# Kernel optimization log

Hardware: AMD Instinct MI355X
Metric: run time of the kernel (lower is better)

The kernel has to match this reference:

```python
import jax, jax.numpy as jnp
import numpy as np

EMBED_DIM = 1024
NUM_HEADS = 16
HEAD_DIM = EMBED_DIM // NUM_HEADS


def setup_inputs() -> dict:
    key = jax.random.key(0)
    k1, k2, k3, k4, k5 = jax.random.split(key, 5)
    C = EMBED_DIM
    x = jax.random.normal(k1, (4, 2048, C), dtype=jnp.float32)
    s = 1.0 / np.sqrt(C)
    qkv_w = jax.random.uniform(k2, (3 * C, C), jnp.float32, -s, s)
    qkv_b = jax.random.uniform(k3, (3 * C,), jnp.float32, -s, s)
    proj_w = jax.random.uniform(k4, (C, C), jnp.float32, -s, s)
    proj_b = jax.random.uniform(k5, (C,), jnp.float32, -s, s)
    return {"x": x, "qkv_w": qkv_w, "qkv_b": qkv_b, "proj_w": proj_w, "proj_b": proj_b}


def reference(x, qkv_w, qkv_b, proj_w, proj_b):
    B, T, C = x.shape
    H, D = NUM_HEADS, HEAD_DIM
    qkv = jnp.einsum('btc,oc->bto', x, qkv_w) + qkv_b  # [B,T,3C]
    q, k, v = jnp.split(qkv, 3, axis=2)
    # [B,T,C] -> [B,H,T,D]
    q = q.reshape(B, T, H, D).transpose(0, 2, 1, 3)
    k = k.reshape(B, T, H, D).transpose(0, 2, 1, 3)
    v = v.reshape(B, T, H, D).transpose(0, 2, 1, 3)
    scores = jnp.einsum('bhqd,bhkd->bhqk', q, k) / jnp.sqrt(jnp.float32(D)).astype(q.dtype)
    causal = jnp.tril(jnp.ones((T, T), dtype=bool))
    scores = jnp.where(causal[None, None], scores, jnp.finfo(scores.dtype).min)
    attn = jax.nn.softmax(scores, axis=-1)
    out = jnp.einsum('bhqk,bhkd->bhqd', attn, v)
    out = out.transpose(0, 2, 1, 3).reshape(B, T, C)
    return jnp.einsum('btc,oc->bto', out, proj_w) + proj_b
```

## Files before the change

kernel.cpp:

```cpp
#include <hip/hip_runtime.h>

#define EMBED 1024
#define C3    3072
#define NHEAD 16
#define HDIM  64
#define BB    4
#define TT    2048
#define MTOK  8192

typedef __bf16 bf16;
typedef __bf16 bf16x4 __attribute__((ext_vector_type(4)));
typedef __bf16 bf16x8 __attribute__((ext_vector_type(8)));
typedef float  f32x4  __attribute__((ext_vector_type(4)));
typedef float  f32x16 __attribute__((ext_vector_type(16)));
typedef unsigned int u32;

__device__ __forceinline__ void gload_lds16(const bf16* g, bf16* l) {
  __builtin_amdgcn_global_load_lds((__attribute__((address_space(1))) void*)g,
                                   (__attribute__((address_space(3))) void*)l,
                                   16, 0, 0);
}

__device__ __forceinline__ u32 pkbf(float lo, float hi_) {
  union { bf16 h[2]; u32 w; } u;
  u.h[0] = (bf16)lo; u.h[1] = (bf16)hi_;
  return u.w;
}

union upw { u32 w[4]; bf16x8 v; };

__global__ __launch_bounds__(256) void cvt_all(const float* __restrict__ x,
                                               const float* __restrict__ w1,
                                               const float* __restrict__ w2,
                                               bf16* __restrict__ xb,
                                               bf16* __restrict__ wqkv,
                                               bf16* __restrict__ wproj) {
  const int N1 = MTOK * EMBED, N2 = C3 * EMBED, N3 = EMBED * EMBED;
  int i = (blockIdx.x * blockDim.x + threadIdx.x) * 4;
  const float* src; bf16* dst;
  if (i < N1)           { src = x + i;            dst = xb + i; }
  else if (i < N1 + N2) { src = w1 + (i - N1);    dst = wqkv + (i - N1); }
  else if (i < N1 + N2 + N3) { src = w2 + (i - N1 - N2); dst = wproj + (i - N1 - N2); }
  else return;
  float4 v = *reinterpret_cast<const float4*>(src);
  bf16x4 o;
  o[0] = (bf16)v.x; o[1] = (bf16)v.y; o[2] = (bf16)v.z; o[3] = (bf16)v.w;
  *reinterpret_cast<bf16x4*>(dst) = o;
}

__device__ __forceinline__ void gemm_core(const bf16* __restrict__ A,
                                          const bf16* __restrict__ W,
                                          int K, int bm0, int bn0,
                                          int wm, int wn, int l15, int lg,
                                          f32x4 (&acc)[4][4]) {
  __shared__ __align__(16) bf16 lA[128 * 64];
  __shared__ __align__(16) bf16 lB[128 * 64];
  const int tid  = threadIdx.x;
  const int grow = tid >> 3;
  const int gseg = tid & 7;

  const bf16* srcA[4];
  const bf16* srcB[4];
#pragma unroll
  for (int r = 0; r < 4; ++r) {
    const int row = r * 32 + grow;
    const int seg = gseg ^ (row & 7);
    srcA[r] = A + (size_t)(bm0 + row) * K + seg * 8;
    srcB[r] = W + (size_t)(bn0 + row) * K + seg * 8;
  }
  int offA[2][4], offB[2][4];
#pragma unroll
  for (int kk = 0; kk < 2; ++kk) {
#pragma unroll
    for (int i = 0; i < 4; ++i) {
      const int rowA = wm + i * 16 + l15;
      const int rowB = wn + i * 16 + l15;
      offA[kk][i] = rowA * 128 + ((kk * 64 + lg * 16) ^ ((rowA & 7) << 4));
      offB[kk][i] = rowB * 128 + ((kk * 64 + lg * 16) ^ ((rowB & 7) << 4));
    }
  }

  for (int kt = 0; kt < K; kt += 64) {
#pragma unroll
    for (int r = 0; r < 4; ++r) {
      gload_lds16(srcA[r] + kt, &lA[(r * 256 + tid) * 8]);
      gload_lds16(srcB[r] + kt, &lB[(r * 256 + tid) * 8]);
    }
    __syncthreads();
    const char* Ab = (const char*)lA;
    const char* Bb = (const char*)lB;
#pragma unroll
    for (int kk = 0; kk < 2; ++kk) {
      bf16x8 af[4], bf_[4];
#pragma unroll
      for (int i = 0; i < 4; ++i) af[i]  = *reinterpret_cast<const bf16x8*>(Ab + offA[kk][i]);
#pragma unroll
      for (int j = 0; j < 4; ++j) bf_[j] = *reinterpret_cast<const bf16x8*>(Bb + offB[kk][j]);
#pragma unroll
      for (int i = 0; i < 4; ++i)
#pragma unroll
        for (int j = 0; j < 4; ++j)
          acc[i][j] = __builtin_amdgcn_mfma_f32_16x16x32_bf16(af[i], bf_[j],
                                                              acc[i][j], 0, 0, 0);
    }
    __syncthreads();
  }
}

__global__ __launch_bounds__(256) void gemm_qkv(const bf16* __restrict__ A,
                                                const bf16* __restrict__ W,
                                                const float* __restrict__ bias,
                                                bf16* __restrict__ Qh,
                                                bf16* __restrict__ Kh,
                                                bf16* __restrict__ VhT) {
  const int tid  = threadIdx.x;
  const int lane = tid & 63, wave = tid >> 6;
  const int wm   = (wave >> 1) * 64;
  const int wn   = (wave & 1) * 64;
  const int bn0  = blockIdx.x * 128;
  const int bm0  = blockIdx.y * 128;
  const int l15  = lane & 15, lg = lane >> 4;

  f32x4 acc[4][4] = {};
  gemm_core(A, W, EMBED, bm0, bn0, wm, wn, l15, lg, acc);

  const int sec = bn0 >> 10;
#pragma unroll
  for (int i = 0; i < 4; ++i)
#pragma unroll
    for (int j = 0; j < 4; ++j) {
      const int col = bn0 + wn + j * 16 + l15;
      const float bs = bias[col];
      const int c2 = col & 1023, hh = c2 >> 6, dd = c2 & 63;
      const int rowb = bm0 + wm + i * 16 + lg * 4;
      const int bb = rowb >> 11, t0 = rowb & 2047;
      const int bh = bb * 16 + hh;
      if (sec < 2) {
        bf16* dst = (sec ? Kh : Qh) + ((size_t)bh * TT + t0) * HDIM + dd;
#pragma unroll
        for (int r = 0; r < 4; ++r) dst[(size_t)r * HDIM] = (bf16)(acc[i][j][r] + bs);
      } else {
        bf16x4 o4;
#pragma unroll
        for (int r = 0; r < 4; ++r) o4[r] = (bf16)(acc[i][j][r] + bs);
        *reinterpret_cast<bf16x4*>(VhT + ((size_t)bh * HDIM + dd) * TT + t0) = o4;
      }
    }
}

__global__ __launch_bounds__(256) void gemm_bt(const bf16* __restrict__ A,
                                               const bf16* __restrict__ W,
                                               const float* __restrict__ bias,
                                               float* __restrict__ Cf,
                                               int M, int N, int K) {
  const int tid  = threadIdx.x;
  const int lane = tid & 63, wave = tid >> 6;
  const int wm   = (wave >> 1) * 64;
  const int wn   = (wave & 1) * 64;
  const int bn0  = blockIdx.x * 128;
  const int bm0  = blockIdx.y * 128;
  const int l15  = lane & 15, lg = lane >> 4;

  f32x4 acc[4][4] = {};
  gemm_core(A, W, K, bm0, bn0, wm, wn, l15, lg, acc);

#pragma unroll
  for (int i = 0; i < 4; ++i)
#pragma unroll
    for (int j = 0; j < 4; ++j) {
      int col = bn0 + wn + j * 16 + l15;
      float bs = bias[col];
#pragma unroll
      for (int r = 0; r < 4; ++r) {
        int row = bm0 + wm + i * 16 + lg * 4 + r;
        Cf[(size_t)row * N + col] = acc[i][j][r] + bs;
      }
    }
}

__device__ __forceinline__ void attn_tile(const char* kbase, const char* vbase,
                                          const bf16x8 (&qfr)[4], f32x16 (&oacc)[2],
                                          float& mrun, float& srun,
                                          const int kv0, const int q0w,
                                          const int l31, const int hi, const int swz) {
  f32x16 s0 = {}, s1 = {};
  __builtin_amdgcn_s_setprio(1);
#pragma unroll
  for (int dc = 0; dc < 4; ++dc) {
    bf16x8 kf = *reinterpret_cast<const bf16x8*>(
        kbase + l31 * 128 + (((2 * dc + hi) * 16) ^ swz));
    s0 = __builtin_amdgcn_mfma_f32_32x32x16_bf16(kf, qfr[dc], s0, 0, 0, 0);
  }
#pragma unroll
  for (int dc = 0; dc < 4; ++dc) {
    bf16x8 kf = *reinterpret_cast<const bf16x8*>(
        kbase + (32 + l31) * 128 + (((2 * dc + hi) * 16) ^ swz));
    s1 = __builtin_amdgcn_mfma_f32_32x32x16_bf16(kf, qfr[dc], s1, 0, 0, 0);
  }
  __builtin_amdgcn_s_setprio(0);

  if (kv0 + 63 > q0w) {
    const int qg = q0w + l31;
#pragma unroll
    for (int r = 0; r < 16; ++r) {
      const int kvb = kv0 + (r & 3) + 8 * (r >> 2) + 4 * hi;
      if (kvb > qg)      s0[r] = -3e38f;
      if (kvb + 32 > qg) s1[r] = -3e38f;
    }
  }

  float m8[8];
#pragma unroll
  for (int i = 0; i < 8; ++i)
    m8[i] = fmaxf(fmaxf(s0[i], s0[i + 8]), fmaxf(s1[i], s1[i + 8]));
#pragma unroll
  for (int st = 4; st > 0; st >>= 1)
#pragma unroll
    for (int i = 0; i < st; ++i) m8[i] = fmaxf(m8[i], m8[i + st]);
  float mx = fmaxf(m8[0], __shfl_xor(m8[0], 32));

  float mref = mrun;
  if (!__all(mx <= mrun + 8.0f)) {
    const float mnew = fmaxf(mrun, mx);
    const float corr = __builtin_amdgcn_exp2f(mrun - mnew);
    mrun = mnew; mref = mnew;
    srun *= corr;
#pragma unroll
    for (int r = 0; r < 16; ++r) { oacc[0][r] *= corr; oacc[1][r] *= corr; }
  }

  float psum = 0.0f;
#pragma unroll
  for (int r = 0; r < 16; ++r) {
    s0[r] = __builtin_amdgcn_exp2f(s0[r] - mref);
    s1[r] = __builtin_amdgcn_exp2f(s1[r] - mref);
    psum += s0[r] + s1[r];
  }
  srun += psum;

  upw pw[4];
#pragma unroll
  for (int cl = 0; cl < 2; ++cl) {
    {
      u32 a01 = pkbf(s0[8 * cl + 0], s0[8 * cl + 1]);
      u32 a23 = pkbf(s0[8 * cl + 2], s0[8 * cl + 3]);
      u32 b01 = pkbf(s0[8 * cl + 4], s0[8 * cl + 5]);
      u32 b23 = pkbf(s0[8 * cl + 6], s0[8 * cl + 7]);
      asm("v_permlane32_swap_b32 %0, %1" : "+v"(a01), "+v"(b01));
      asm("v_permlane32_swap_b32 %0, %1" : "+v"(a23), "+v"(b23));
      pw[cl].w[0] = a01; pw[cl].w[1] = a23; pw[cl].w[2] = b01; pw[cl].w[3] = b23;
    }
    {
      u32 a01 = pkbf(s1[8 * cl + 0], s1[8 * cl + 1]);
      u32 a23 = pkbf(s1[8 * cl + 2], s1[8 * cl + 3]);
      u32 b01 = pkbf(s1[8 * cl + 4], s1[8 * cl + 5]);
      u32 b23 = pkbf(s1[8 * cl + 6], s1[8 * cl + 7]);
      asm("v_permlane32_swap_b32 %0, %1" : "+v"(a01), "+v"(b01));
      asm("v_permlane32_swap_b32 %0, %1" : "+v"(a23), "+v"(b23));
      pw[2 + cl].w[0] = a01; pw[2 + cl].w[1] = a23; pw[2 + cl].w[2] = b01; pw[2 + cl].w[3] = b23;
    }
  }

  __builtin_amdgcn_s_setprio(1);
#pragma unroll
  for (int dh = 0; dh < 2; ++dh) {
    const char* vrow = vbase + (32 * dh + l31) * 128;
#pragma unroll
    for (int c = 0; c < 4; ++c) {
      bf16x8 vf = *reinterpret_cast<const bf16x8*>(vrow + (((2 * c + hi) * 16) ^ swz));
      oacc[dh] = __builtin_amdgcn_mfma_f32_32x32x16_bf16(vf, pw[c].v, oacc[dh], 0, 0, 0);
    }
  }
  __builtin_amdgcn_s_setprio(0);
}

__global__ __launch_bounds__(256, 2) void attn_kernel(const bf16* __restrict__ Qh,
                                                      const bf16* __restrict__ Kh,
                                                      const bf16* __restrict__ VhT,
                                                      bf16* __restrict__ aout) {
  __shared__ __align__(16) bf16 lK[2][64 * 64];
  __shared__ __align__(16) bf16 lVT[2][64 * 64];
  const int tid  = threadIdx.x;
  const int lane = tid & 63, wave = tid >> 6;
  const int l31  = lane & 31;
  const int hi   = lane >> 5;
  const int bid  = blockIdx.x;
  const int bh   = bid & 63;
  const int p    = bid >> 6;
  const int qtH  = 15 - p, qtL = p;
  const int b    = bh >> 4, h = bh & 15;
  const int q0H  = qtH * 128 + wave * 32;
  const int q0L  = qtL * 128 + wave * 32;
  const size_t tb = (size_t)b * TT;
  const int swz  = (l31 & 7) << 4;

  const float QSCALE = 0.18033688011112042f;
  bf16x8 qfrH[4], qfrL[4];
  {
    const bf16* qrowH = Qh + ((size_t)bh * TT + q0H + l31) * HDIM;
    const bf16* qrowL = Qh + ((size_t)bh * TT + q0L + l31) * HDIM;
#pragma unroll
    for (int dc = 0; dc < 4; ++dc) {
      bf16x8 vH = *reinterpret_cast<const bf16x8*>(qrowH + dc * 16 + hi * 8);
      bf16x8 vL = *reinterpret_cast<const bf16x8*>(qrowL + dc * 16 + hi * 8);
      bf16x8 oH, oL;
#pragma unroll
      for (int j = 0; j < 8; ++j) {
        oH[j] = (bf16)((float)vH[j] * QSCALE);
        oL[j] = (bf16)((float)vL[j] * QSCALE);
      }
      qfrH[dc] = oH; qfrL[dc] = oL;
    }
  }

  f32x16 oaccH[2] = {}, oaccL[2] = {};
  float mH = -3e38f, sH = 0.0f, mL = -3e38f, sL = 0.0f;

  const int r0 = tid >> 3, sg = tid & 7;
  const bf16* kS0 = Kh + ((size_t)bh * TT + r0) * HDIM + (size_t)(sg ^ (r0 & 7)) * 8;
  const bf16* kS1 = Kh + ((size_t)bh * TT + 32 + r0) * HDIM + (size_t)(sg ^ (r0 & 7)) * 8;
  const bf16* vS0 = VhT + ((size_t)bh * HDIM + r0) * TT + (size_t)(sg ^ (r0 & 7)) * 8;
  const bf16* vS1 = VhT + ((size_t)bh * HDIM + 32 + r0) * TT + (size_t)(sg ^ (r0 & 7)) * 8;

  const int nkv = 2 * qtH + 2;

  gload_lds16(kS0, &lK[0][tid * 8]);
  gload_lds16(kS1, &lK[0][(tid + 256) * 8]);
  gload_lds16(vS0, &lVT[0][tid * 8]);
  gload_lds16(vS1, &lVT[0][(tid + 256) * 8]);
  __syncthreads();

  int cur = 0;
  for (int t = 0; t < nkv; ++t) {
    const int kv0 = t * 64;
    if (t + 1 < nkv) {
      const int kvn = kv0 + 64;
      gload_lds16(kS0 + (size_t)kvn * HDIM, &lK[cur ^ 1][tid * 8]);
      gload_lds16(kS1 + (size_t)kvn * HDIM, &lK[cur ^ 1][(tid + 256) * 8]);
      gload_lds16(vS0 + kvn, &lVT[cur ^ 1][tid * 8]);
      gload_lds16(vS1 + kvn, &lVT[cur ^ 1][(tid + 256) * 8]);
    }

    const char* kbase = (const char*)&lK[cur][0];
    const char* vbase = (const char*)&lVT[cur][0];
    if (kv0 <= q0H + 31)
      attn_tile(kbase, vbase, qfrH, oaccH, mH, sH, kv0, q0H, l31, hi, swz);
    if (kv0 <= q0L + 31)
      attn_tile(kbase, vbase, qfrL, oaccL, mL, sL, kv0, q0L, l31, hi, swz);

    __syncthreads();
    cur ^= 1;
  }

#pragma unroll
  for (int band = 0; band < 2; ++band) {
    const f32x16* oacc = band ? oaccL : oaccH;
    float sr = band ? sL : sH;
    sr += __shfl_xor(sr, 32);
    const float inv = 1.0f / sr;
    const int q = (band ? q0L : q0H) + l31;
    bf16* orow = aout + (tb + q) * (size_t)EMBED + h * HDIM;
#pragma unroll
    for (int dh = 0; dh < 2; ++dh)
#pragma unroll
      for (int rb = 0; rb < 4; ++rb) {
        bf16x4 o4;
#pragma unroll
        for (int k = 0; k < 4; ++k) o4[k] = (bf16)(oacc[dh][4 * rb + k] * inv);
        *reinterpret_cast<bf16x4*>(orow + 32 * dh + 8 * rb + 4 * hi) = o4;
      }
  }
}

extern "C" void kernel_launch(void* const* d_in, const int* in_sizes, int n_in,
                              void* d_out, int out_size, void* d_ws, size_t ws_size,
                              hipStream_t stream) {
  const float* x      = (const float*)d_in[0];
  const float* qkv_w  = (const float*)d_in[1];
  const float* qkv_b  = (const float*)d_in[2];
  const float* proj_w = (const float*)d_in[3];
  const float* proj_b = (const float*)d_in[4];
  float* out = (float*)d_out;

  const size_t QSZ = (size_t)BB * NHEAD * TT * HDIM;
  char* ws = (char*)d_ws;
  bf16* xb    = (bf16*)ws;
  bf16* wqkv  = xb + (size_t)MTOK * EMBED;
  bf16* wproj = wqkv + (size_t)C3 * EMBED;
  bf16* Qh    = wproj + (size_t)EMBED * EMBED;
  bf16* Kh    = Qh + QSZ;
  bf16* VhT   = Kh + QSZ;
  bf16* aob   = xb;

  const int NCVT = (MTOK * EMBED + C3 * EMBED + EMBED * EMBED) / 4;
  cvt_all<<<dim3((NCVT + 255) / 256), dim3(256), 0, stream>>>(x, qkv_w, proj_w,
                                                              xb, wqkv, wproj);

  gemm_qkv<<<dim3(C3 / 128, MTOK / 128), dim3(256), 0, stream>>>(xb, wqkv, qkv_b, Qh, Kh, VhT);

  attn_kernel<<<dim3(512), dim3(256), 0, stream>>>(Qh, Kh, VhT, aob);

  gemm_bt<<<dim3(EMBED / 128, MTOK / 128), dim3(256), 0, stream>>>(
      aob, wproj, proj_b, out, MTOK, EMBED, EMBED);
}
```

Baseline: 165.7 us.

## Split attention blocks into two 64-row halves with 128 threads each

Each attention block now has 2 waves instead of 4 and covers 64 query rows per band, so the grid doubles to 1024 blocks. The K/V tile loads are reorganized so 128 threads issue four 16-row groups per buffer. The goal is more blocks to fill the GPU's compute units and finer load balancing across the causal workload. In exchange, each K/V tile is loaded from global memory twice as often, since two blocks now share each query tile.

```diff
diff --git a/kernel.cpp b/kernel.cpp
--- a/kernel.cpp
+++ b/kernel.cpp
@@ -274,7 +274,7 @@
   __builtin_amdgcn_s_setprio(0);
 }
 
-__global__ __launch_bounds__(256, 2) void attn_kernel(const bf16* __restrict__ Qh,
+__global__ __launch_bounds__(128, 2) void attn_kernel(const bf16* __restrict__ Qh,
                                                       const bf16* __restrict__ Kh,
                                                       const bf16* __restrict__ VhT,
                                                       bf16* __restrict__ aout) {
@@ -285,12 +285,13 @@
   const int l31  = lane & 31;
   const int hi   = lane >> 5;
   const int bid  = blockIdx.x;
-  const int bh   = bid & 63;
-  const int p    = bid >> 6;
+  const int qh   = bid & 1;
+  const int bh   = (bid >> 1) & 63;
+  const int p    = bid >> 7;
   const int qtH  = 15 - p, qtL = p;
   const int b    = bh >> 4, h = bh & 15;
-  const int q0H  = qtH * 128 + wave * 32;
-  const int q0L  = qtL * 128 + wave * 32;
+  const int q0H  = qtH * 128 + qh * 64 + wave * 32;
+  const int q0L  = qtL * 128 + qh * 64 + wave * 32;
   const size_t tb = (size_t)b * TT;
   const int swz  = (l31 & 7) << 4;
 
@@ -316,18 +317,24 @@
   f32x16 oaccH[2] = {}, oaccL[2] = {};
   float mH = -3e38f, sH = 0.0f, mL = -3e38f, sL = 0.0f;
 
-  const int r0 = tid >> 3, sg = tid & 7;
-  const bf16* kS0 = Kh + ((size_t)bh * TT + r0) * HDIM + (size_t)(sg ^ (r0 & 7)) * 8;
-  const bf16* kS1 = Kh + ((size_t)bh * TT + 32 + r0) * HDIM + (size_t)(sg ^ (r0 & 7)) * 8;
-  const bf16* vS0 = VhT + ((size_t)bh * HDIM + r0) * TT + (size_t)(sg ^ (r0 & 7)) * 8;
-  const bf16* vS1 = VhT + ((size_t)bh * HDIM + 32 + r0) * TT + (size_t)(sg ^ (r0 & 7)) * 8;
+  const int r0 = tid >> 3;
+  const int sg = tid & 7;
+  const int seg = sg ^ (r0 & 7);
+  const bf16* kS[4];
+  const bf16* vS[4];
+#pragma unroll
+  for (int g = 0; g < 4; ++g) {
+    kS[g] = Kh + ((size_t)bh * TT + g * 16 + r0) * HDIM + seg * 8;
+    vS[g] = VhT + ((size_t)bh * HDIM + g * 16 + r0) * TT + seg * 8;
+  }
 
   const int nkv = 2 * qtH + 2;
 
-  gload_lds16(kS0, &lK[0][tid * 8]);
-  gload_lds16(kS1, &lK[0][(tid + 256) * 8]);
-  gload_lds16(vS0, &lVT[0][tid * 8]);
-  gload_lds16(vS1, &lVT[0][(tid + 256) * 8]);
+#pragma unroll
+  for (int g = 0; g < 4; ++g) {
+    gload_lds16(kS[g], &lK[0][(g * 128 + tid) * 8]);
+    gload_lds16(vS[g], &lVT[0][(g * 128 + tid) * 8]);
+  }
   __syncthreads();
 
   int cur = 0;
@@ -335,10 +342,11 @@
     const int kv0 = t * 64;
     if (t + 1 < nkv) {
       const int kvn = kv0 + 64;
-      gload_lds16(kS0 + (size_t)kvn * HDIM, &lK[cur ^ 1][tid * 8]);
-      gload_lds16(kS1 + (size_t)kvn * HDIM, &lK[cur ^ 1][(tid + 256) * 8]);
-      gload_lds16(vS0 + kvn, &lVT[cur ^ 1][tid * 8]);
-      gload_lds16(vS1 + kvn, &lVT[cur ^ 1][(tid + 256) * 8]);
+#pragma unroll
+      for (int g = 0; g < 4; ++g) {
+        gload_lds16(kS[g] + (size_t)kvn * HDIM, &lK[cur ^ 1][(g * 128 + tid) * 8]);
+        gload_lds16(vS[g] + kvn, &lVT[cur ^ 1][(g * 128 + tid) * 8]);
+      }
     }
 
     const char* kbase = (const char*)&lK[cur][0];
@@ -398,7 +406,7 @@
 
   gemm_qkv<<<dim3(C3 / 128, MTOK / 128), dim3(256), 0, stream>>>(xb, wqkv, qkv_b, Qh, Kh, VhT);
 
-  attn_kernel<<<dim3(512), dim3(256), 0, stream>>>(Qh, Kh, VhT, aob);
+  attn_kernel<<<dim3(1024), dim3(128), 0, stream>>>(Qh, Kh, VhT, aob);
 
   gemm_bt<<<dim3(EMBED / 128, MTOK / 128), dim3(256), 0, stream>>>(
       aob, wproj, proj_b, out, MTOK, EMBED, EMBED);
```

Result: no change. 168.8 us (+1.8%).

## Software-pipeline attention so QK of next tile overlaps softmax and PV

Applied to the files above, without the earlier changes.

Splits the per-tile attention work into a QK MFMA stage and a softmax/PV stage. Each iteration computes the scores for tile t while finishing softmax and the PV product for tile t-1, using ping-pong score registers. The K/V LDS ring grows from two to four slots so tile t-1's V stays valid while later tiles are staged. The aim is to hide the softmax latency behind matrix-core work, at the cost of twice the LDS per block and many more live score VGPRs, which may cause spills or lower occupancy.

```diff
diff --git a/kernel.cpp b/kernel.cpp
--- a/kernel.cpp
+++ b/kernel.cpp
@@ -178,27 +178,32 @@
     }
 }
 
-__device__ __forceinline__ void attn_tile(const char* kbase, const char* vbase,
-                                          const bf16x8 (&qfr)[4], f32x16 (&oacc)[2],
-                                          float& mrun, float& srun,
-                                          const int kv0, const int q0w,
-                                          const int l31, const int hi, const int swz) {
-  f32x16 s0 = {}, s1 = {};
+__device__ __forceinline__ void load_kf(const char* kbase, bf16x8 (&kf0)[4], bf16x8 (&kf1)[4],
+                                        int l31, int hi, int swz) {
+#pragma unroll
+  for (int dc = 0; dc < 4; ++dc) {
+    kf0[dc] = *reinterpret_cast<const bf16x8*>(kbase + l31 * 128 + (((2 * dc + hi) * 16) ^ swz));
+    kf1[dc] = *reinterpret_cast<const bf16x8*>(kbase + (32 + l31) * 128 + (((2 * dc + hi) * 16) ^ swz));
+  }
+}
+
+__device__ __forceinline__ void qk_one(const bf16x8 (&kf0)[4], const bf16x8 (&kf1)[4],
+                                       const bf16x8 (&qfr)[4], f32x16& s0, f32x16& s1) {
+  f32x16 a = {}, b = {};
   __builtin_amdgcn_s_setprio(1);
 #pragma unroll
   for (int dc = 0; dc < 4; ++dc) {
-    bf16x8 kf = *reinterpret_cast<const bf16x8*>(
-        kbase + l31 * 128 + (((2 * dc + hi) * 16) ^ swz));
-    s0 = __builtin_amdgcn_mfma_f32_32x32x16_bf16(kf, qfr[dc], s0, 0, 0, 0);
-  }
-#pragma unroll
-  for (int dc = 0; dc < 4; ++dc) {
-    bf16x8 kf = *reinterpret_cast<const bf16x8*>(
-        kbase + (32 + l31) * 128 + (((2 * dc + hi) * 16) ^ swz));
-    s1 = __builtin_amdgcn_mfma_f32_32x32x16_bf16(kf, qfr[dc], s1, 0, 0, 0);
+    a = __builtin_amdgcn_mfma_f32_32x32x16_bf16(kf0[dc], qfr[dc], a, 0, 0, 0);
+    b = __builtin_amdgcn_mfma_f32_32x32x16_bf16(kf1[dc], qfr[dc], b, 0, 0, 0);
   }
   __builtin_amdgcn_s_setprio(0);
-
+  s0 = a; s1 = b;
+}
+
+__device__ __forceinline__ void fin_band(const char* vbase, f32x16& s0, f32x16& s1,
+                                         f32x16 (&oacc)[2], float& mrun, float& srun,
+                                         const int kv0, const int q0w,
+                                         const int l31, const int hi, const int swz) {
   if (kv0 + 63 > q0w) {
     const int qg = q0w + l31;
 #pragma unroll
@@ -208,7 +213,6 @@
       if (kvb + 32 > qg) s1[r] = -3e38f;
     }
   }
-
   float m8[8];
 #pragma unroll
   for (int i = 0; i < 8; ++i)
@@ -274,12 +278,21 @@
   __builtin_amdgcn_s_setprio(0);
 }
 
+__device__ __forceinline__ void stage_tile(const bf16* kS0, const bf16* kS1,
+                                           const bf16* vS0, const bf16* vS1,
+                                           int kv, bf16* kb, bf16* vb, int tid) {
+  gload_lds16(kS0 + (size_t)kv * HDIM, kb + tid * 8);
+  gload_lds16(kS1 + (size_t)kv * HDIM, kb + (tid + 256) * 8);
+  gload_lds16(vS0 + kv, vb + tid * 8);
+  gload_lds16(vS1 + kv, vb + (tid + 256) * 8);
+}
+
 __global__ __launch_bounds__(256, 2) void attn_kernel(const bf16* __restrict__ Qh,
                                                       const bf16* __restrict__ Kh,
                                                       const bf16* __restrict__ VhT,
                                                       bf16* __restrict__ aout) {
-  __shared__ __align__(16) bf16 lK[2][64 * 64];
-  __shared__ __align__(16) bf16 lVT[2][64 * 64];
+  __shared__ __align__(16) bf16 lK[4][64 * 64];
+  __shared__ __align__(16) bf16 lVT[4][64 * 64];
   const int tid  = threadIdx.x;
   const int lane = tid & 63, wave = tid >> 6;
   const int l31  = lane & 31;
@@ -314,7 +327,7 @@
   }
 
   f32x16 oaccH[2] = {}, oaccL[2] = {};
-  float mH = -3e38f, sH = 0.0f, mL = -3e38f, sL = 0.0f;
+  float mH = -3e38f, sHr = 0.0f, mL = -3e38f, sLr = 0.0f;
 
   const int r0 = tid >> 3, sg = tid & 7;
   const bf16* kS0 = Kh + ((size_t)bh * TT + r0) * HDIM + (size_t)(sg ^ (r0 & 7)) * 8;
@@ -324,38 +337,62 @@
 
   const int nkv = 2 * qtH + 2;
 
-  gload_lds16(kS0, &lK[0][tid * 8]);
-  gload_lds16(kS1, &lK[0][(tid + 256) * 8]);
-  gload_lds16(vS0, &lVT[0][tid * 8]);
-  gload_lds16(vS1, &lVT[0][(tid + 256) * 8]);
+  f32x16 sAh0, sAh1, sAl0, sAl1;
+  f32x16 sBh0, sBh1, sBl0, sBl1;
+
+#define HALF_ITER(T, NH0, NH1, NL0, NL1, OH0, OH1, OL0, OL1)                              \
+  do {                                                                                    \
+    const int t_ = (T);                                                                   \
+    if (t_ + 1 < nkv)                                                                     \
+      stage_tile(kS0, kS1, vS0, vS1, (t_ + 1) * 64,                                       \
+                 &lK[(t_ + 1) & 3][0], &lVT[(t_ + 1) & 3][0], tid);                       \
+    {                                                                                     \
+      const char* vb_ = (const char*)&lVT[(t_ - 1) & 3][0];                               \
+      const int pk_ = (t_ - 1) * 64;                                                      \
+      fin_band(vb_, OH0, OH1, oaccH, mH, sHr, pk_, q0H, l31, hi, swz);                    \
+      if (pk_ <= q0L + 31)                                                                \
+        fin_band(vb_, OL0, OL1, oaccL, mL, sLr, pk_, q0L, l31, hi, swz);                  \
+    }                                                                                     \
+    {                                                                                     \
+      const char* kb_ = (const char*)&lK[t_ & 3][0];                                      \
+      bf16x8 kf0_[4], kf1_[4];                                                            \
+      load_kf(kb_, kf0_, kf1_, l31, hi, swz);                                             \
+      qk_one(kf0_, kf1_, qfrH, NH0, NH1);                                                 \
+      if (t_ * 64 <= q0L + 31) qk_one(kf0_, kf1_, qfrL, NL0, NL1);                        \
+    }                                                                                     \
+    __syncthreads();                                                                      \
+  } while (0)
+
+  stage_tile(kS0, kS1, vS0, vS1, 0, &lK[0][0], &lVT[0][0], tid);
   __syncthreads();
-
-  int cur = 0;
-  for (int t = 0; t < nkv; ++t) {
-    const int kv0 = t * 64;
-    if (t + 1 < nkv) {
-      const int kvn = kv0 + 64;
-      gload_lds16(kS0 + (size_t)kvn * HDIM, &lK[cur ^ 1][tid * 8]);
-      gload_lds16(kS1 + (size_t)kvn * HDIM, &lK[cur ^ 1][(tid + 256) * 8]);
-      gload_lds16(vS0 + kvn, &lVT[cur ^ 1][tid * 8]);
-      gload_lds16(vS1 + kvn, &lVT[cur ^ 1][(tid + 256) * 8]);
-    }
-
-    const char* kbase = (const char*)&lK[cur][0];
-    const char* vbase = (const char*)&lVT[cur][0];
-    if (kv0 <= q0H + 31)
-      attn_tile(kbase, vbase, qfrH, oaccH, mH, sH, kv0, q0H, l31, hi, swz);
-    if (kv0 <= q0L + 31)
-      attn_tile(kbase, vbase, qfrL, oaccL, mL, sL, kv0, q0L, l31, hi, swz);
-
+  {
+    stage_tile(kS0, kS1, vS0, vS1, 64, &lK[1][0], &lVT[1][0], tid);
+    bf16x8 kf0_[4], kf1_[4];
+    load_kf((const char*)&lK[0][0], kf0_, kf1_, l31, hi, swz);
+    qk_one(kf0_, kf1_, qfrH, sAh0, sAh1);
+    qk_one(kf0_, kf1_, qfrL, sAl0, sAl1);
     __syncthreads();
-    cur ^= 1;
-  }
+  }
+
+  int t = 1;
+  for (; t + 1 < nkv; t += 2) {
+    HALF_ITER(t,     sBh0, sBh1, sBl0, sBl1, sAh0, sAh1, sAl0, sAl1);
+    HALF_ITER(t + 1, sAh0, sAh1, sAl0, sAl1, sBh0, sBh1, sBl0, sBl1);
+  }
+  HALF_ITER(t, sBh0, sBh1, sBl0, sBl1, sAh0, sAh1, sAl0, sAl1);
+  {
+    const char* vb_ = (const char*)&lVT[(nkv - 1) & 3][0];
+    const int pk_ = (nkv - 1) * 64;
+    fin_band(vb_, sBh0, sBh1, oaccH, mH, sHr, pk_, q0H, l31, hi, swz);
+    if (pk_ <= q0L + 31)
+      fin_band(vb_, sBl0, sBl1, oaccL, mL, sLr, pk_, q0L, l31, hi, swz);
+  }
+#undef HALF_ITER
 
 #pragma unroll
   for (int band = 0; band < 2; ++band) {
     const f32x16* oacc = band ? oaccL : oaccH;
-    float sr = band ? sL : sH;
+    float sr = band ? sLr : sHr;
     sr += __shfl_xor(sr, 32);
     const float inv = 1.0f / sr;
     const int q = (band ? q0L : q0H) + l31;
```

Result: slower. 202.7 us (+22.3%).

## Double-buffer GEMM LDS tiles with split prefetch and MFMA priority

Applied to the files above, without the earlier changes.

Turns the shared GEMM core into a double-buffered pipeline. Global-to-LDS loads for the next K tile are issued in two halves interleaved with the MFMA work on the current tile, using explicit vmcnt waits and raw barriers. MFMA sections are also wrapped in s_setprio. This aims to hide global load latency behind compute, at the cost of twice the LDS per block, which may lower occupancy, plus delicate hand-written wait counts.

```diff
diff --git a/kernel.cpp b/kernel.cpp
--- a/kernel.cpp
+++ b/kernel.cpp
@@ -53,8 +53,8 @@
                                           int K, int bm0, int bn0,
                                           int wm, int wn, int l15, int lg,
                                           f32x4 (&acc)[4][4]) {
-  __shared__ __align__(16) bf16 lA[128 * 64];
-  __shared__ __align__(16) bf16 lB[128 * 64];
+  __shared__ __align__(16) bf16 lA[2][128 * 64];
+  __shared__ __align__(16) bf16 lB[2][128 * 64];
   const int tid  = threadIdx.x;
   const int grow = tid >> 3;
   const int gseg = tid & 7;
@@ -80,30 +80,59 @@
     }
   }
 
-  for (int kt = 0; kt < K; kt += 64) {
-#pragma unroll
-    for (int r = 0; r < 4; ++r) {
-      gload_lds16(srcA[r] + kt, &lA[(r * 256 + tid) * 8]);
-      gload_lds16(srcB[r] + kt, &lB[(r * 256 + tid) * 8]);
-    }
-    __syncthreads();
-    const char* Ab = (const char*)lA;
-    const char* Bb = (const char*)lB;
+  const int nt = K >> 6;
+#pragma unroll
+  for (int r = 0; r < 4; ++r) {
+    gload_lds16(srcA[r], &lA[0][(r * 256 + tid) * 8]);
+    gload_lds16(srcB[r], &lB[0][(r * 256 + tid) * 8]);
+  }
+
+  for (int t = 0; t < nt; ++t) {
+    const int cur = t & 1;
+    const int kt1 = (t + 1) << 6;
+    const bool pf = (t + 1 < nt);
+
+    if (pf) {
+#pragma unroll
+      for (int r = 0; r < 2; ++r) {
+        gload_lds16(srcA[r] + kt1, &lA[cur ^ 1][(r * 256 + tid) * 8]);
+        gload_lds16(srcB[r] + kt1, &lB[cur ^ 1][(r * 256 + tid) * 8]);
+      }
+      asm volatile("s_waitcnt vmcnt(4)" ::: "memory");
+    } else {
+      asm volatile("s_waitcnt vmcnt(0)" ::: "memory");
+    }
+    __builtin_amdgcn_sched_barrier(0);
+    __builtin_amdgcn_s_barrier();
+    __builtin_amdgcn_sched_barrier(0);
+
+    const char* Ab = (const char*)&lA[cur][0];
+    const char* Bb = (const char*)&lB[cur][0];
 #pragma unroll
     for (int kk = 0; kk < 2; ++kk) {
+      if (kk == 1 && pf) {
+#pragma unroll
+        for (int r = 2; r < 4; ++r) {
+          gload_lds16(srcA[r] + kt1, &lA[cur ^ 1][(r * 256 + tid) * 8]);
+          gload_lds16(srcB[r] + kt1, &lB[cur ^ 1][(r * 256 + tid) * 8]);
+        }
+      }
       bf16x8 af[4], bf_[4];
 #pragma unroll
       for (int i = 0; i < 4; ++i) af[i]  = *reinterpret_cast<const bf16x8*>(Ab + offA[kk][i]);
 #pragma unroll
       for (int j = 0; j < 4; ++j) bf_[j] = *reinterpret_cast<const bf16x8*>(Bb + offB[kk][j]);
+      __builtin_amdgcn_s_setprio(1);
 #pragma unroll
       for (int i = 0; i < 4; ++i)
 #pragma unroll
         for (int j = 0; j < 4; ++j)
           acc[i][j] = __builtin_amdgcn_mfma_f32_16x16x32_bf16(af[i], bf_[j],
                                                               acc[i][j], 0, 0, 0);
-    }
-    __syncthreads();
+      __builtin_amdgcn_s_setprio(0);
+    }
+    __builtin_amdgcn_s_barrier();
+    __builtin_amdgcn_sched_barrier(0);
   }
 }
 
```

New measurement: 181.1 us. +9.3%, slower.
